# Kernel tuning notes

Hardware: AMD Instinct MI355X
Metric: run time of the kernel (lower is better)

The kernel has to match this reference:

```python
import jax, jax.numpy as jnp
import numpy as np

T, B, DIN, H = 2048, 64, 512, 512


def setup_inputs() -> dict:
    key = jax.random.key(0)
    ks = jax.random.split(key, 5)
    s = 1.0 / np.sqrt(H)
    return {
        "X": jax.random.normal(ks[0], (T, B, DIN), dtype=jnp.float32),
        "Wx": jax.random.normal(ks[1], (DIN, 4 * H), dtype=jnp.float32) * s,
        "bx": jax.random.normal(ks[2], (4 * H,), dtype=jnp.float32) * s,
        "Wh": jax.random.normal(ks[3], (H, 4 * H), dtype=jnp.float32) * s,
        "bh": jax.random.normal(ks[4], (4 * H,), dtype=jnp.float32) * s,
    }


def reference(X, Wx, bx, Wh, bh):
    # Precompute input projections for all timesteps in one big GEMM
    # (same math as 4 per-step W_* linears, gate order [i, f, o, z]).
    x_proj = jnp.einsum('tbd,dg->tbg', X, Wx) + bx  # [T, B, 4H]
    h0 = jnp.zeros((B, H), dtype=X.dtype)
    c0 = jnp.zeros((B, H), dtype=X.dtype)

    def step(carry, xp):
        h, c, h_sum, c_sum = carry
        g = xp + h @ Wh + bh                       # [B, 4H]
        i_g, f_g, o_g, z_g = jnp.split(g, 4, axis=-1)
        i = jax.nn.sigmoid(i_g)
        f = jax.nn.sigmoid(f_g)
        o = jax.nn.sigmoid(o_g)
        z = jnp.tanh(z_g)
        c_t = i * z + f * c
        h_t = o * jnp.tanh(c_t)
        return (h_t, c_t, h_sum + h_t, c_sum + c_t), None

    (_, _, h_sum, c_sum), _ = jax.lax.scan(step, (h0, c0, h0, c0), x_proj)
    inv_T = jnp.asarray(1.0 / T, dtype=X.dtype)
    return h_sum * inv_T, c_sum * inv_T
```

## Files before the change

### kernel.cpp

```cpp
#include <hip/hip_runtime.h>
#include <hip/hip_bf16.h>
#include <stdint.h>


#define TSTEPS 2048
#define BATCH  64
#define DINK   512
#define HHH    512
#define GB     4
#define GC     16
#define ROWS   16
#define NTHR   256

typedef __attribute__((ext_vector_type(8))) short  short8;
typedef __attribute__((ext_vector_type(4))) float  float4v;
typedef __attribute__((ext_vector_type(4))) int    int4v;

static __device__ __forceinline__ unsigned short f2bf(float f) {
    union { float f; unsigned u; } v; v.f = f;
    unsigned u = v.u + 0x7FFFu + ((v.u >> 16) & 1u);
    return (unsigned short)(u >> 16);
}
static __device__ __forceinline__ float sigm(float x) {
    return 1.0f / (1.0f + __expf(-x));
}
static __device__ __forceinline__ float tanh_fast(float x) {
    return 2.0f / (1.0f + __expf(-2.0f * x)) - 1.0f;
}

__global__ __launch_bounds__(NTHR, 1) void lstm_scan(
    const float* __restrict__ X,
    const float* __restrict__ Wx,
    const float* __restrict__ bx,
    const float* __restrict__ Wh,
    const float* __restrict__ bh,
    float* out,
    unsigned short* hbuf,
    unsigned* sync)
{
    __shared__ float P[4][ROWS][132];
    __shared__ float cst[ROWS][33];
    __shared__ float hsum[ROWS][33];
    __shared__ float csum[ROWS][33];
    __shared__ float biasLds[128];

    const int tid  = threadIdx.x;
    const int wv   = tid >> 6;
    const int lane = tid & 63;
    const int l15  = lane & 15;
    const int quad = lane >> 4;
    const int g    = blockIdx.x >> 4;
    const int wc   = blockIdx.x & 15;
    const int rb   = g * ROWS;
    const int jbase = wc * 32;

    unsigned* slots = sync + g * 64;

    const float* Wsrc = (wv < 2) ? Wx : Wh;
    const int k0 = (wv & 1) * 256;
    short8 bfrag[8][8];
    #pragma unroll
    for (int kc = 0; kc < 8; ++kc) {
        #pragma unroll
        for (int nt = 0; nt < 8; ++nt) {
            const int c    = nt * 16 + l15;
            const int gcol = (c >> 5) * HHH + jbase + (c & 31);
            const int kl   = k0 + kc * 32 + quad * 8;
            short8 tmp;
            #pragma unroll
            for (int j = 0; j < 8; ++j)
                tmp[j] = (short)f2bf(Wsrc[(size_t)(kl + j) * 2048 + gcol]);
            bfrag[kc][nt] = tmp;
        }
    }
    if (tid < 128) {
        const int gcol = (tid >> 5) * HHH + jbase + (tid & 31);
        biasLds[tid] = bx[gcol] + bh[gcol];
    }
    for (int i = tid; i < ROWS * 33; i += NTHR) {
        (&cst[0][0])[i] = 0.f; (&hsum[0][0])[i] = 0.f; (&csum[0][0])[i] = 0.f;
    }
    __syncthreads();

    const int r_ew  = tid >> 4;
    const int jj_ew = (tid & 15) * 2;

    for (int t = 0; t < TSTEPS; ++t) {
        const unsigned short* hR = hbuf + ((t + 1) & 1) * (BATCH * HHH);
        unsigned short*       hW = hbuf + (t & 1)       * (BATCH * HHH);

        float4v acc[8];
        #pragma unroll
        for (int nt = 0; nt < 8; ++nt) acc[nt] = (float4v){0.f, 0.f, 0.f, 0.f};

        if (wv < 2) {
            const float* xrow = X + (size_t)t * (BATCH * DINK)
                                  + (size_t)(rb + l15) * DINK + k0 + quad * 8;
            int4v xv[16];
            #define XLOAD(i, OFF) asm volatile( \
                "global_load_dwordx4 %0, %1, off offset:" OFF \
                : "=v"(xv[i]) : "v"(xrow))
            XLOAD( 0, "0");    XLOAD( 1, "16");
            XLOAD( 2, "128");  XLOAD( 3, "144");
            XLOAD( 4, "256");  XLOAD( 5, "272");
            XLOAD( 6, "384");  XLOAD( 7, "400");
            XLOAD( 8, "512");  XLOAD( 9, "528");
            XLOAD(10, "640");  XLOAD(11, "656");
            XLOAD(12, "768");  XLOAD(13, "784");
            XLOAD(14, "896");  XLOAD(15, "912");
            #undef XLOAD
            asm volatile("s_waitcnt vmcnt(8)"
                : "+v"(xv[0]), "+v"(xv[1]), "+v"(xv[2]), "+v"(xv[3]),
                  "+v"(xv[4]), "+v"(xv[5]), "+v"(xv[6]), "+v"(xv[7]));
            #pragma unroll
            for (int kc = 0; kc < 4; ++kc) {
                union { int4v i; float4v f; } a0, a1;
                a0.i = xv[2 * kc]; a1.i = xv[2 * kc + 1];
                short8 av;
                av[0] = (short)f2bf(a0.f[0]); av[1] = (short)f2bf(a0.f[1]);
                av[2] = (short)f2bf(a0.f[2]); av[3] = (short)f2bf(a0.f[3]);
                av[4] = (short)f2bf(a1.f[0]); av[5] = (short)f2bf(a1.f[1]);
                av[6] = (short)f2bf(a1.f[2]); av[7] = (short)f2bf(a1.f[3]);
                #pragma unroll
                for (int nt = 0; nt < 8; ++nt)
                    acc[nt] = __builtin_amdgcn_mfma_f32_16x16x32_bf16(
                        av, bfrag[kc][nt], acc[nt], 0, 0, 0);
            }
            asm volatile("s_waitcnt vmcnt(0)"
                : "+v"(xv[8]),  "+v"(xv[9]),  "+v"(xv[10]), "+v"(xv[11]),
                  "+v"(xv[12]), "+v"(xv[13]), "+v"(xv[14]), "+v"(xv[15]));
            #pragma unroll
            for (int kc = 4; kc < 8; ++kc) {
                union { int4v i; float4v f; } a0, a1;
                a0.i = xv[2 * kc]; a1.i = xv[2 * kc + 1];
                short8 av;
                av[0] = (short)f2bf(a0.f[0]); av[1] = (short)f2bf(a0.f[1]);
                av[2] = (short)f2bf(a0.f[2]); av[3] = (short)f2bf(a0.f[3]);
                av[4] = (short)f2bf(a1.f[0]); av[5] = (short)f2bf(a1.f[1]);
                av[6] = (short)f2bf(a1.f[2]); av[7] = (short)f2bf(a1.f[3]);
                #pragma unroll
                for (int nt = 0; nt < 8; ++nt)
                    acc[nt] = __builtin_amdgcn_mfma_f32_16x16x32_bf16(
                        av, bfrag[kc][nt], acc[nt], 0, 0, 0);
            }
        } else {
            if (t > 0) {
                for (;;) {
                    unsigned v = __hip_atomic_load(slots + lane, __ATOMIC_RELAXED,
                                                   __HIP_MEMORY_SCOPE_AGENT);
                    if (__all((int)(v >= (unsigned)t))) break;
                }
                __builtin_amdgcn_fence(__ATOMIC_ACQUIRE, "workgroup");
            }
            const int hc0 = (wv - 2) * 256;
            const unsigned short* hrow = hR + (size_t)(rb + l15) * HHH + hc0 + quad * 8;
            int4v hv[8];
            #define HLOAD(i, OFF) asm volatile( \
                "global_load_dwordx4 %0, %1, off offset:" OFF " sc0 sc1" \
                : "=v"(hv[i]) : "v"(hrow))
            HLOAD(0, "0");   HLOAD(1, "64");  HLOAD(2, "128"); HLOAD(3, "192");
            HLOAD(4, "256"); HLOAD(5, "320"); HLOAD(6, "384"); HLOAD(7, "448");
            #undef HLOAD
            asm volatile("s_waitcnt vmcnt(0)"
                : "+v"(hv[0]), "+v"(hv[1]), "+v"(hv[2]), "+v"(hv[3]),
                  "+v"(hv[4]), "+v"(hv[5]), "+v"(hv[6]), "+v"(hv[7]));
            #pragma unroll
            for (int kc = 0; kc < 8; ++kc) {
                union { int4v i; short8 s; } u; u.i = hv[kc];
                #pragma unroll
                for (int nt = 0; nt < 8; ++nt)
                    acc[nt] = __builtin_amdgcn_mfma_f32_16x16x32_bf16(
                        u.s, bfrag[kc][nt], acc[nt], 0, 0, 0);
            }
        }

        #pragma unroll
        for (int nt = 0; nt < 8; ++nt) {
            const int col = nt * 16 + l15;
            #pragma unroll
            for (int r = 0; r < 4; ++r)
                P[wv][quad * 4 + r][col] = acc[nt][r];
        }
        __syncthreads();

        {
            float h2[2];
            #pragma unroll
            for (int e = 0; e < 2; ++e) {
                const int jj = jj_ew + e;
                const int r  = r_ew;
                float gi = biasLds[jj]      + P[0][r][jj]      + P[1][r][jj]      + P[2][r][jj]      + P[3][r][jj];
                float gf = biasLds[32 + jj] + P[0][r][32 + jj] + P[1][r][32 + jj] + P[2][r][32 + jj] + P[3][r][32 + jj];
                float go = biasLds[64 + jj] + P[0][r][64 + jj] + P[1][r][64 + jj] + P[2][r][64 + jj] + P[3][r][64 + jj];
                float gz = biasLds[96 + jj] + P[0][r][96 + jj] + P[1][r][96 + jj] + P[2][r][96 + jj] + P[3][r][96 + jj];
                const float c_old = cst[r][jj];
                const float cn = sigm(gi) * tanh_fast(gz) + sigm(gf) * c_old;
                const float hn = sigm(go) * tanh_fast(cn);
                cst[r][jj]  = cn;
                csum[r][jj] += cn;
                hsum[r][jj] += hn;
                h2[e] = hn;
            }
            const unsigned pk = (unsigned)f2bf(h2[0]) | ((unsigned)f2bf(h2[1]) << 16);
            unsigned* dst = (unsigned*)(hW + (size_t)(rb + r_ew) * HHH + jbase + jj_ew);
            __hip_atomic_store(dst, pk, __ATOMIC_RELAXED, __HIP_MEMORY_SCOPE_AGENT);
        }

        asm volatile("s_waitcnt vmcnt(0)" ::: "memory");
        if (lane == 0)
            __hip_atomic_store(slots + (wc * 4 + wv), (unsigned)(t + 1),
                               __ATOMIC_RELAXED, __HIP_MEMORY_SCOPE_AGENT);

        __syncthreads();
    }

    {
        unsigned* base = sync + wv * 64 + lane;
        for (;;) {
            unsigned v = __hip_atomic_load(base, __ATOMIC_RELAXED, __HIP_MEMORY_SCOPE_AGENT);
            if (__all((int)(v >= (unsigned)TSTEPS))) break;
        }
    }
    __syncthreads();

    const float invT = 1.0f / (float)TSTEPS;
    {
        const int b = rb + r_ew;
        const size_t o0 = (size_t)b * HHH + jbase + jj_ew;
        out[o0]                              = hsum[r_ew][jj_ew] * invT;
        out[o0 + 1]                          = hsum[r_ew][jj_ew + 1] * invT;
        out[(size_t)(BATCH * HHH) + o0]      = csum[r_ew][jj_ew] * invT;
        out[(size_t)(BATCH * HHH) + o0 + 1]  = csum[r_ew][jj_ew + 1] * invT;
    }
}

extern "C" void kernel_launch(void* const* d_in, const int* in_sizes, int n_in,
                              void* d_out, int out_size, void* d_ws, size_t ws_size,
                              hipStream_t stream) {
    (void)in_sizes; (void)n_in; (void)out_size;
    const float* X  = (const float*)d_in[0];
    const float* Wx = (const float*)d_in[1];
    const float* bx = (const float*)d_in[2];
    const float* Wh = (const float*)d_in[3];
    const float* bh = (const float*)d_in[4];
    float* out = (float*)d_out;

    const size_t HBUF_BYTES = (size_t)2 * BATCH * HHH * 2;
    const size_t SYNC_BYTES = 4096;
    char* scratch = (ws_size >= HBUF_BYTES + SYNC_BYTES) ? (char*)d_ws : (char*)d_out;
    unsigned short* hbuf = (unsigned short*)scratch;
    unsigned* sync = (unsigned*)(scratch + HBUF_BYTES);

    hipMemsetAsync(scratch, 0, HBUF_BYTES + SYNC_BYTES, stream);
    lstm_scan<<<GB * GC, NTHR, 0, stream>>>(X, Wx, bx, Wh, bh, out, hbuf, sync);
}
```

Before: 9.444 ms.

## Replace flag-based step barrier with timestep-tagged hidden-state words

Each bf16 hidden value is stored in a 32-bit word whose upper 16 bits carry the timestep tag. Consumers poll the h data directly until every tag reaches the current step, which removes the separate flag store, the vmcnt wait before it, and the extra flag-load round trip. In exchange the h traffic doubles and each poll reloads the full row. The 16-bit tag wraps only at 65536, so it is safe for 2048 steps. The final all-blocks barrier is dropped and the buffer moves to a device global symbol.

```diff
diff --git a/kernel.cpp b/kernel.cpp
--- a/kernel.cpp
+++ b/kernel.cpp
@@ -12,9 +12,12 @@
 #define ROWS   16
 #define NTHR   256
 
-typedef __attribute__((ext_vector_type(8))) short  short8;
-typedef __attribute__((ext_vector_type(4))) float  float4v;
-typedef __attribute__((ext_vector_type(4))) int    int4v;
+typedef __attribute__((ext_vector_type(8))) short    short8;
+typedef __attribute__((ext_vector_type(4))) float    float4v;
+typedef __attribute__((ext_vector_type(4))) int      int4v;
+typedef __attribute__((ext_vector_type(2))) unsigned uint2v;
+
+__device__ __attribute__((aligned(16))) unsigned g_hbuf[2 * BATCH * HHH];
 
 static __device__ __forceinline__ unsigned short f2bf(float f) {
     union { float f; unsigned u; } v; v.f = f;
@@ -26,6 +29,9 @@
 }
 static __device__ __forceinline__ float tanh_fast(float x) {
     return 2.0f / (1.0f + __expf(-2.0f * x)) - 1.0f;
+}
+static __device__ __forceinline__ unsigned umin2(unsigned a, unsigned b) {
+    return a < b ? a : b;
 }
 
 __global__ __launch_bounds__(NTHR, 1) void lstm_scan(
@@ -35,8 +41,7 @@
     const float* __restrict__ Wh,
     const float* __restrict__ bh,
     float* out,
-    unsigned short* hbuf,
-    unsigned* sync)
+    unsigned* hbuf)
 {
     __shared__ float P[4][ROWS][132];
     __shared__ float cst[ROWS][33];
@@ -53,8 +58,6 @@
     const int wc   = blockIdx.x & 15;
     const int rb   = g * ROWS;
     const int jbase = wc * 32;
-
-    unsigned* slots = sync + g * 64;
 
     const float* Wsrc = (wv < 2) ? Wx : Wh;
     const int k0 = (wv & 1) * 256;
@@ -86,8 +89,8 @@
     const int jj_ew = (tid & 15) * 2;
 
     for (int t = 0; t < TSTEPS; ++t) {
-        const unsigned short* hR = hbuf + ((t + 1) & 1) * (BATCH * HHH);
-        unsigned short*       hW = hbuf + (t & 1)       * (BATCH * HHH);
+        const unsigned* hRu = hbuf + ((t + 1) & 1) * (BATCH * HHH);
+        unsigned*       hWu = hbuf + (t & 1)       * (BATCH * HHH);
 
         float4v acc[8];
         #pragma unroll
@@ -144,33 +147,51 @@
                         av, bfrag[kc][nt], acc[nt], 0, 0, 0);
             }
         } else {
-            if (t > 0) {
-                for (;;) {
-                    unsigned v = __hip_atomic_load(slots + lane, __ATOMIC_RELAXED,
-                                                   __HIP_MEMORY_SCOPE_AGENT);
-                    if (__all((int)(v >= (unsigned)t))) break;
+            const int hc0 = (wv - 2) * 256;
+            const unsigned* hrow = hRu + (size_t)(rb + l15) * HHH + hc0 + quad * 8;
+            const unsigned thr = (unsigned)t << 16;
+            int4v hv[16];
+            for (;;) {
+                #define HLOAD(i, OFF) asm volatile( \
+                    "global_load_dwordx4 %0, %1, off offset:" OFF " sc0 sc1" \
+                    : "=v"(hv[i]) : "v"(hrow))
+                HLOAD( 0, "0");    HLOAD( 1, "16");
+                HLOAD( 2, "128");  HLOAD( 3, "144");
+                HLOAD( 4, "256");  HLOAD( 5, "272");
+                HLOAD( 6, "384");  HLOAD( 7, "400");
+                HLOAD( 8, "512");  HLOAD( 9, "528");
+                HLOAD(10, "640");  HLOAD(11, "656");
+                HLOAD(12, "768");  HLOAD(13, "784");
+                HLOAD(14, "896");  HLOAD(15, "912");
+                #undef HLOAD
+                asm volatile("s_waitcnt vmcnt(0)"
+                    : "+v"(hv[0]),  "+v"(hv[1]),  "+v"(hv[2]),  "+v"(hv[3]),
+                      "+v"(hv[4]),  "+v"(hv[5]),  "+v"(hv[6]),  "+v"(hv[7]),
+                      "+v"(hv[8]),  "+v"(hv[9]),  "+v"(hv[10]), "+v"(hv[11]),
+                      "+v"(hv[12]), "+v"(hv[13]), "+v"(hv[14]), "+v"(hv[15]));
+                if (t == 0) break;
+                unsigned m = 0xFFFFFFFFu;
+                #pragma unroll
+                for (int i = 0; i < 16; ++i) {
+                    union { int4v v; unsigned u[4]; } q; q.v = hv[i];
+                    m = umin2(m, umin2(umin2(q.u[0], q.u[1]),
+                                       umin2(q.u[2], q.u[3])));
                 }
-                __builtin_amdgcn_fence(__ATOMIC_ACQUIRE, "workgroup");
-            }
-            const int hc0 = (wv - 2) * 256;
-            const unsigned short* hrow = hR + (size_t)(rb + l15) * HHH + hc0 + quad * 8;
-            int4v hv[8];
-            #define HLOAD(i, OFF) asm volatile( \
-                "global_load_dwordx4 %0, %1, off offset:" OFF " sc0 sc1" \
-                : "=v"(hv[i]) : "v"(hrow))
-            HLOAD(0, "0");   HLOAD(1, "64");  HLOAD(2, "128"); HLOAD(3, "192");
-            HLOAD(4, "256"); HLOAD(5, "320"); HLOAD(6, "384"); HLOAD(7, "448");
-            #undef HLOAD
-            asm volatile("s_waitcnt vmcnt(0)"
-                : "+v"(hv[0]), "+v"(hv[1]), "+v"(hv[2]), "+v"(hv[3]),
-                  "+v"(hv[4]), "+v"(hv[5]), "+v"(hv[6]), "+v"(hv[7]));
+                if (__all((int)(m >= thr))) break;
+            }
             #pragma unroll
             for (int kc = 0; kc < 8; ++kc) {
-                union { int4v i; short8 s; } u; u.i = hv[kc];
+                union { int4v v; unsigned u[4]; } a0, a1;
+                a0.v = hv[2 * kc]; a1.v = hv[2 * kc + 1];
+                short8 av;
+                av[0] = (short)(a0.u[0] & 0xFFFFu); av[1] = (short)(a0.u[1] & 0xFFFFu);
+                av[2] = (short)(a0.u[2] & 0xFFFFu); av[3] = (short)(a0.u[3] & 0xFFFFu);
+                av[4] = (short)(a1.u[0] & 0xFFFFu); av[5] = (short)(a1.u[1] & 0xFFFFu);
+                av[6] = (short)(a1.u[2] & 0xFFFFu); av[7] = (short)(a1.u[3] & 0xFFFFu);
                 #pragma unroll
                 for (int nt = 0; nt < 8; ++nt)
                     acc[nt] = __builtin_amdgcn_mfma_f32_16x16x32_bf16(
-                        u.s, bfrag[kc][nt], acc[nt], 0, 0, 0);
+                        av, bfrag[kc][nt], acc[nt], 0, 0, 0);
             }
         }
 
@@ -201,27 +222,17 @@
                 hsum[r][jj] += hn;
                 h2[e] = hn;
             }
-            const unsigned pk = (unsigned)f2bf(h2[0]) | ((unsigned)f2bf(h2[1]) << 16);
-            unsigned* dst = (unsigned*)(hW + (size_t)(rb + r_ew) * HHH + jbase + jj_ew);
-            __hip_atomic_store(dst, pk, __ATOMIC_RELAXED, __HIP_MEMORY_SCOPE_AGENT);
-        }
-
-        asm volatile("s_waitcnt vmcnt(0)" ::: "memory");
-        if (lane == 0)
-            __hip_atomic_store(slots + (wc * 4 + wv), (unsigned)(t + 1),
-                               __ATOMIC_RELAXED, __HIP_MEMORY_SCOPE_AGENT);
+            const unsigned tagW = ((unsigned)(t + 1)) << 16;
+            uint2v pk;
+            pk[0] = tagW | (unsigned)f2bf(h2[0]);
+            pk[1] = tagW | (unsigned)f2bf(h2[1]);
+            unsigned* dst = hWu + (size_t)(rb + r_ew) * HHH + jbase + jj_ew;
+            asm volatile("global_store_dwordx2 %0, %1, off sc0 sc1"
+                         :: "v"(dst), "v"(pk) : "memory");
+        }
 
         __syncthreads();
     }
-
-    {
-        unsigned* base = sync + wv * 64 + lane;
-        for (;;) {
-            unsigned v = __hip_atomic_load(base, __ATOMIC_RELAXED, __HIP_MEMORY_SCOPE_AGENT);
-            if (__all((int)(v >= (unsigned)TSTEPS))) break;
-        }
-    }
-    __syncthreads();
 
     const float invT = 1.0f / (float)TSTEPS;
     {
@@ -245,12 +256,13 @@
     const float* bh = (const float*)d_in[4];
     float* out = (float*)d_out;
 
-    const size_t HBUF_BYTES = (size_t)2 * BATCH * HHH * 2;
-    const size_t SYNC_BYTES = 4096;
-    char* scratch = (ws_size >= HBUF_BYTES + SYNC_BYTES) ? (char*)d_ws : (char*)d_out;
-    unsigned short* hbuf = (unsigned short*)scratch;
-    unsigned* sync = (unsigned*)(scratch + HBUF_BYTES);
-
-    hipMemsetAsync(scratch, 0, HBUF_BYTES + SYNC_BYTES, stream);
-    lstm_scan<<<GB * GC, NTHR, 0, stream>>>(X, Wx, bx, Wh, bh, out, hbuf, sync);
-}
+    const size_t HBUF_BYTES = sizeof(unsigned) * 2 * BATCH * HHH;
+
+    static void* sym = nullptr;
+    if (!sym) hipGetSymbolAddress(&sym, HIP_SYMBOL(g_hbuf));
+    unsigned* hbuf = sym ? (unsigned*)sym
+                         : (ws_size >= HBUF_BYTES ? (unsigned*)d_ws : (unsigned*)d_out);
+
+    hipMemsetAsync(hbuf, 0, HBUF_BYTES, stream);
+    lstm_scan<<<GB * GC, NTHR, 0, stream>>>(X, Wx, bx, Wh, bh, out, hbuf);
+}
```

Result: faster. 9.087 ms (-3.8%).
